# Performance work log

Hardware: AMD Instinct MI355X
Metric: run time of the kernel (lower is better)

## Reference

```python
import jax, jax.numpy as jnp
import numpy as np
from jax import lax

P = 8  # DFFN patch_size


def _ln(x, w, b):
    # WithBias LayerNorm over channel dim of NCHW (matches to_3d -> LN(-1) -> to_4d)
    mu = x.mean(1, keepdims=True)
    var = ((x - mu) ** 2).mean(1, keepdims=True)
    return (x - mu) / jnp.sqrt(var + 1e-5) * w[None, :, None, None] + b[None, :, None, None]


def _conv1x1(x, w, b=None):
    y = jnp.einsum('bchw,oc->bohw', x, w)
    if b is not None:
        y = y + b[None, :, None, None]
    return y


def setup_inputs() -> dict:
    key = jax.random.key(0)
    ks = jax.random.split(key, 9)
    B, C, H, W = 2, 64, 96, 96
    hid = C  # ffn_expansion_factor = 1
    s = lambda k, shape, scale=0.05: jax.random.normal(k, shape, jnp.float32) * scale
    return {
        'x': s(ks[0], (B, C, H, W), 1.0),
        'ln1_w': jnp.ones((C,), jnp.float32), 'ln1_b': jnp.zeros((C,), jnp.float32),
        'ln2_w': jnp.ones((C,), jnp.float32), 'ln2_b': jnp.zeros((C,), jnp.float32),
        'q_w': s(ks[1], (C, C)), 'q_b': jnp.zeros((C,), jnp.float32),
        'k_w': s(ks[2], (C, C)), 'k_b': jnp.zeros((C,), jnp.float32),
        'v_w': s(ks[3], (C, C)), 'v_b': jnp.zeros((C,), jnp.float32),
        'fft_w': s(ks[4], (hid, P, P // 2 + 1), 1.0),
        'proj_in_w': s(ks[5], (hid, C)),
        'dw_w': s(ks[6], (hid, 1, 3, 3)),
        'proj_out_w': s(ks[7], (C, hid // 2)),
    }


def reference(x, ln1_w, ln1_b, ln2_w, ln2_b, q_w, q_b, k_w, k_b, v_w, v_b,
              fft_w, proj_in_w, dw_w, proj_out_w):
    B, C, H, W = x.shape
    # --- attention sub-block (unscaled spatial self-attn) ---
    xn = _ln(x, ln1_w, ln1_b)
    q = _conv1x1(xn, q_w, q_b).reshape(B, C, H * W)
    k = _conv1x1(xn, k_w, k_b).reshape(B, C, H * W)
    v = _conv1x1(xn, v_w, v_b).reshape(B, C, H * W)
    attn = jax.nn.softmax(jnp.einsum('bcn,bcm->bnm', q, k), axis=-1)  # [B, HW, HW]
    out = jnp.einsum('bcm,bnm->bcn', v, attn).reshape(B, C, H, W)
    x = x + out
    # --- DFFN sub-block ---
    xn = _ln(x, ln2_w, ln2_b)
    h = _conv1x1(xn, proj_in_w)  # hidden == C (expansion factor 1)
    hid = h.shape[1]
    hb, wb = H // P, W // P
    hp = h.reshape(B, hid, hb, P, wb, P).transpose(0, 2, 4, 1, 3, 5)  # [B,hb,wb,hid,P,P]
    hf = jnp.fft.rfft2(hp) * fft_w  # real learned spectral filter
    hp = jnp.fft.irfft2(hf, s=(P, P))
    h = hp.transpose(0, 3, 1, 4, 2, 5).reshape(B, hid, H, W)
    h = lax.conv_general_dilated(h, dw_w, (1, 1), ((1, 1), (1, 1)),
                                 feature_group_count=hid,
                                 dimension_numbers=('NCHW', 'OIHW', 'NCHW'))
    h1, h2 = jnp.split(h, 2, axis=1)
    h = jax.nn.gelu(h1, approximate=False) * h2  # torch F.gelu is exact erf
    return x + _conv1x1(h, proj_out_w)
```

## Files before the change

kernel.cpp:

```cpp
#include <hip/hip_runtime.h>
#include <hip/hip_bf16.h>
#include <math.h>

#define CH 64
#define NPOS 9216
#define NTOT 18432
#define NSPLIT 12
#define TILES_PER_SPLIT 12
#define LOG2E 1.4426950408889634f

typedef short bf16x8 __attribute__((ext_vector_type(8)));
typedef short bf16x4 __attribute__((ext_vector_type(4)));
typedef float f32x4 __attribute__((ext_vector_type(4)));
typedef int   i32x4 __attribute__((ext_vector_type(4)));
typedef int   i32x2 __attribute__((ext_vector_type(2)));
typedef unsigned int u32;

__device__ __forceinline__ float bf2f(short s) {
  unsigned int u = ((unsigned int)(unsigned short)s) << 16;
  return __builtin_bit_cast(float, u);
}
__device__ __forceinline__ short f2bf(float f) {
  unsigned int u = __builtin_bit_cast(unsigned int, f);
  unsigned int r = (u + 0x7fffu + ((u >> 16) & 1u)) >> 16;
  return (short)r;
}
__device__ __forceinline__ float gelu_exact(float x) {
  return 0.5f * x * (1.f + erff(x * 0.70710678118654752440f));
}


__global__ __launch_bounds__(256) void k_ln_qkv(
    const float* __restrict__ x, const float* __restrict__ ln1w, const float* __restrict__ ln1b,
    const float* __restrict__ qw, const float* __restrict__ qb,
    const float* __restrict__ kw, const float* __restrict__ kb,
    const float* __restrict__ vw, const float* __restrict__ vb,
    short* __restrict__ Qg, short* __restrict__ Kg, short* __restrict__ Vgt) {
  int mat = blockIdx.y;
  int half = blockIdx.z;
  const float* wsrc = (mat == 0) ? qw : (mat == 1) ? kw : vw;
  const float* bsrc = (mat == 0) ? qb : (mat == 1) ? kb : vb;
  int idx = blockIdx.x * 256 + threadIdx.x;
  int b = idx / NPOS, n = idx % NPOS;
  const float* xb = x + (size_t)b * CH * NPOS + n;
  float xr[64];
  float mu = 0.f;
#pragma unroll
  for (int c = 0; c < 64; ++c) { float v = xb[c * NPOS]; xr[c] = v; mu += v; }
  mu *= (1.f / 64.f);
  float var = 0.f;
#pragma unroll
  for (int c = 0; c < 64; ++c) { float d = xr[c] - mu; var += d * d; }
  float rstd = rsqrtf(var * (1.f / 64.f) + 1e-5f);
#pragma unroll
  for (int c = 0; c < 64; ++c) xr[c] = (xr[c] - mu) * rstd * ln1w[c] + ln1b[c];
  if (mat == 2) {
    for (int o2 = 0; o2 < 4; ++o2) {
#pragma unroll
      for (int j = 0; j < 8; ++j) {
        int o = half * 32 + o2 * 8 + j;
        float acc = bsrc[o];
        const float* wrow = wsrc + o * 64;
#pragma unroll
        for (int c = 0; c < 64; ++c) acc += wrow[c] * xr[c];
        Vgt[(size_t)o * NTOT + idx] = f2bf(acc);
      }
    }
  } else {
    float kscale = (mat == 1) ? LOG2E : 1.f;
    short* outp = ((mat == 0) ? Qg : Kg) + (size_t)idx * 64 + half * 32;
    for (int o2 = 0; o2 < 4; ++o2) {
      bf16x8 v8;
#pragma unroll
      for (int j = 0; j < 8; ++j) {
        int o = half * 32 + o2 * 8 + j;
        float acc = bsrc[o];
        const float* wrow = wsrc + o * 64;
#pragma unroll
        for (int c = 0; c < 64; ++c) acc += wrow[c] * xr[c];
        v8[j] = f2bf(acc * kscale);
      }
      *(bf16x8*)(outp + o2 * 8) = v8;
    }
  }
}

#define LDPK 80
#define LDP  72
__global__ __launch_bounds__(512) void k_attn(
    const short* __restrict__ Qg, const short* __restrict__ Kg, const short* __restrict__ Vgt,
    u32* __restrict__ PoT, float* __restrict__ Pl) {
  __shared__ __align__(16) short Kt[2][64 * LDPK];
  __shared__ __align__(16) short Vt[2][64 * LDP];
  int b = blockIdx.y;
  int n0 = blockIdx.x * 256;
  int ks = blockIdx.z;
  int tid = threadIdx.x;
  int w = tid >> 6, lane = tid & 63;
  int L = lane & 15, quad = lane >> 4;

  bf16x8 qa[2][2];
#pragma unroll
  for (int qt = 0; qt < 2; ++qt) {
    const short* qb_ = Qg + ((size_t)(b * NPOS + n0 + w * 32 + qt * 16 + L)) * 64;
    qa[qt][0] = *(const bf16x8*)(qb_ + quad * 8);
    qa[qt][1] = *(const bf16x8*)(qb_ + 32 + quad * 8);
  }

  f32x4 o[2][4];
#pragma unroll
  for (int qt = 0; qt < 2; ++qt)
#pragma unroll
    for (int nb = 0; nb < 4; ++nb) o[qt][nb] = (f32x4){0.f, 0.f, 0.f, 0.f};
  float rl[2] = {0.f, 0.f};

  int ck = tid & 7, rk = tid >> 3;
  int c8 = tid & 7, dr = tid >> 3;
  int vslot = (c8 >> 2) * 32 + (c8 & 1) * 16 + ((c8 >> 1) & 1) * 4;
  i32x4 kr, vr;
  {
    int kt = ks * TILES_PER_SPLIT;
    kr = ((const i32x4*)(Kg + ((size_t)(b * NPOS + kt * 64)) * 64))[tid];
    vr = *(const i32x4*)(Vgt + (size_t)b * NPOS + kt * 64 + c8 * 8 + (size_t)dr * NTOT);
    ((i32x4*)Kt[0])[rk * 10 + ck] = kr;
    short* vrow = Vt[0] + dr * LDP + vslot;
    *(i32x2*)(vrow) = (i32x2){vr[0], vr[1]};
    *(i32x2*)(vrow + 8) = (i32x2){vr[2], vr[3]};
  }

  for (int t = 0; t < TILES_PER_SPLIT; ++t) {
    int cur = t & 1;
    if (t + 1 < TILES_PER_SPLIT) {
      int kt = ks * TILES_PER_SPLIT + t + 1;
      kr = ((const i32x4*)(Kg + ((size_t)(b * NPOS + kt * 64)) * 64))[tid];
      vr = *(const i32x4*)(Vgt + (size_t)b * NPOS + kt * 64 + c8 * 8 + (size_t)dr * NTOT);
    }
    __syncthreads();

    const i32x4* kt4 = (const i32x4*)Kt[cur];
    const short* vt = Vt[cur];
    __builtin_amdgcn_s_setprio(1);
#pragma unroll
    for (int kp = 0; kp < 2; ++kp) {
      u32 pw0[4], pw1[4];
#pragma unroll
      for (int h = 0; h < 2; ++h) {
        int kti = kp * 2 + h;
        bf16x8 kf0 = __builtin_bit_cast(bf16x8, kt4[(kti * 16 + L) * 10 + quad]);
        bf16x8 kf1 = __builtin_bit_cast(bf16x8, kt4[(kti * 16 + L) * 10 + 4 + quad]);
#pragma unroll
        for (int qt = 0; qt < 2; ++qt) {
          f32x4 st = {0.f, 0.f, 0.f, 0.f};
          st = __builtin_amdgcn_mfma_f32_16x16x32_bf16(kf0, qa[qt][0], st, 0, 0, 0);
          st = __builtin_amdgcn_mfma_f32_16x16x32_bf16(kf1, qa[qt][1], st, 0, 0, 0);
          float p0 = __builtin_amdgcn_exp2f(st[0]);
          float p1 = __builtin_amdgcn_exp2f(st[1]);
          float p2 = __builtin_amdgcn_exp2f(st[2]);
          float p3 = __builtin_amdgcn_exp2f(st[3]);
          rl[qt] += (p0 + p1) + (p2 + p3);
          u32 lo = __builtin_amdgcn_perm(__builtin_bit_cast(u32, p1), __builtin_bit_cast(u32, p0), 0x07060302u);
          u32 hi = __builtin_amdgcn_perm(__builtin_bit_cast(u32, p3), __builtin_bit_cast(u32, p2), 0x07060302u);
          if (qt == 0) { pw0[h * 2] = lo; pw0[h * 2 + 1] = hi; }
          else         { pw1[h * 2] = lo; pw1[h * 2 + 1] = hi; }
        }
      }
      i32x4 pq0 = {(int)pw0[0], (int)pw0[1], (int)pw0[2], (int)pw0[3]};
      i32x4 pq1 = {(int)pw1[0], (int)pw1[1], (int)pw1[2], (int)pw1[3]};
      bf16x8 pp0 = __builtin_bit_cast(bf16x8, pq0);
      bf16x8 pp1 = __builtin_bit_cast(bf16x8, pq1);
#pragma unroll
      for (int nb = 0; nb < 4; ++nb) {
        bf16x8 va8 = *(const bf16x8*)(vt + (nb * 16 + L) * LDP + kp * 32 + quad * 8);
        o[0][nb] = __builtin_amdgcn_mfma_f32_16x16x32_bf16(va8, pp0, o[0][nb], 0, 0, 0);
        o[1][nb] = __builtin_amdgcn_mfma_f32_16x16x32_bf16(va8, pp1, o[1][nb], 0, 0, 0);
      }
    }
    __builtin_amdgcn_s_setprio(0);

    if (t + 1 < TILES_PER_SPLIT) {
      int nxt = 1 - cur;
      ((i32x4*)Kt[nxt])[rk * 10 + ck] = kr;
      short* vrow = Vt[nxt] + dr * LDP + vslot;
      *(i32x2*)(vrow) = (i32x2){vr[0], vr[1]};
      *(i32x2*)(vrow + 8) = (i32x2){vr[2], vr[3]};
    }
  }

#pragma unroll
  for (int qt = 0; qt < 2; ++qt) {
    rl[qt] += __shfl_xor(rl[qt], 16);
    rl[qt] += __shfl_xor(rl[qt], 32);
  }

#pragma unroll
  for (int qt = 0; qt < 2; ++qt) {
    int qg = b * NPOS + n0 + w * 32 + qt * 16 + L;
#pragma unroll
    for (int nb = 0; nb < 4; ++nb)
#pragma unroll
      for (int ip = 0; ip < 2; ++ip) {
        u32 pk = ((u32)(unsigned short)f2bf(o[qt][nb][2 * ip + 1]) << 16) |
                 (u32)(unsigned short)f2bf(o[qt][nb][2 * ip]);
        int d32 = nb * 8 + quad * 2 + ip;
        PoT[((size_t)(ks * 32 + d32)) * NTOT + qg] = pk;
      }
    if (quad == 0) Pl[(size_t)ks * NTOT + qg] = rl[qt];
  }
}

__global__ __launch_bounds__(256) void k_res_ln2_proj(
    const float* __restrict__ x, const u32* __restrict__ PoT, const float* __restrict__ Pl,
    const float* __restrict__ ln2w, const float* __restrict__ ln2b,
    const float* __restrict__ piw,
    float* __restrict__ X2, float* __restrict__ Hbuf) {
  __shared__ float s1a[256], s2a[256];
  __shared__ __align__(16) short xn[32 * 72];
  int t = threadIdx.x;
  int w8 = t >> 5;
  int p = t & 31;
  int q0 = blockIdx.x * 32;
  int q = q0 + p;
  int b = q / NPOS;
  int nn = q0 % NPOS;
  int n = q % NPOS;

  float lsum = 0.f;
#pragma unroll
  for (int s = 0; s < NSPLIT; ++s) lsum += Pl[(size_t)s * NTOT + q];
  float inv = 1.f / lsum;

  const float* xb = x + (size_t)b * CH * NPOS + n;
  float xr[8];
  float s1 = 0.f, s2 = 0.f;
#pragma unroll
  for (int j2 = 0; j2 < 4; ++j2) {
    float a0 = 0.f, a1 = 0.f;
#pragma unroll
    for (int s = 0; s < NSPLIT; ++s) {
      u32 v = PoT[((size_t)(s * 32 + w8 * 4 + j2)) * NTOT + q];
      a0 += __builtin_bit_cast(float, v << 16);
      a1 += __builtin_bit_cast(float, v & 0xffff0000u);
    }
    int cl = 2 * j2;
    int c = w8 * 8 + cl;
    float v0 = xb[(size_t)c * NPOS] + a0 * inv;
    float v1 = xb[(size_t)(c + 1) * NPOS] + a1 * inv;
    xr[cl] = v0; xr[cl + 1] = v1;
    s1 += v0 + v1;
    s2 += v0 * v0 + v1 * v1;
  }
  s1a[w8 * 32 + p] = s1;
  s2a[w8 * 32 + p] = s2;
  {
    float* xo = X2 + (size_t)b * CH * NPOS + n;
#pragma unroll
    for (int cl = 0; cl < 8; ++cl) xo[(size_t)(w8 * 8 + cl) * NPOS] = xr[cl];
  }
  __syncthreads();
  float mu = 0.f, m2 = 0.f;
#pragma unroll
  for (int ww = 0; ww < 8; ++ww) { mu += s1a[ww * 32 + p]; m2 += s2a[ww * 32 + p]; }
  mu *= (1.f / 64.f);
  float var = m2 * (1.f / 64.f) - mu * mu;
  float rstd = rsqrtf(var + 1e-5f);
  {
    u32* xw = (u32*)xn;
#pragma unroll
    for (int j2 = 0; j2 < 4; ++j2) {
      int cl = 2 * j2, c = w8 * 8 + cl;
      float y0 = (xr[cl] - mu) * rstd * ln2w[c] + ln2b[c];
      float y1 = (xr[cl + 1] - mu) * rstd * ln2w[c + 1] + ln2b[c + 1];
      u32 pk = ((u32)(unsigned short)f2bf(y1) << 16) | (u32)(unsigned short)f2bf(y0);
      xw[p * 36 + w8 * 4 + j2] = pk;
    }
  }
  __syncthreads();
  int lane = t & 63;
  int L = lane & 15, quad = lane >> 4;
  int cs = t >> 6;
  bf16x8 a0, a1;
  {
    const float* wr = piw + (cs * 16 + L) * 64 + quad * 8;
#pragma unroll
    for (int j = 0; j < 8; ++j) { a0[j] = f2bf(wr[j]); a1[j] = f2bf(wr[32 + j]); }
  }
  float* hb = Hbuf + (size_t)b * CH * NPOS + nn;
#pragma unroll
  for (int ps = 0; ps < 2; ++ps) {
    bf16x8 b0 = *(const bf16x8*)(xn + (ps * 16 + L) * 72 + quad * 8);
    bf16x8 b1 = *(const bf16x8*)(xn + (ps * 16 + L) * 72 + 32 + quad * 8);
    f32x4 acc = {0.f, 0.f, 0.f, 0.f};
    acc = __builtin_amdgcn_mfma_f32_16x16x32_bf16(a0, b0, acc, 0, 0, 0);
    acc = __builtin_amdgcn_mfma_f32_16x16x32_bf16(a1, b1, acc, 0, 0, 0);
#pragma unroll
    for (int i = 0; i < 4; ++i)
      hb[(size_t)(cs * 16 + quad * 4 + i) * NPOS + ps * 16 + L] = acc[i];
  }
}

#define LDB 100
__global__ __launch_bounds__(96) void k_conv(
    float* __restrict__ Hbuf, const float* __restrict__ fftw) {
  __shared__ __align__(16) float band[8 * LDB];
  __shared__ float kl[64];
  int hb = blockIdx.x, c = blockIdx.y, b = blockIdx.z;
  int t = threadIdx.x;
  float* base = Hbuf + (size_t)(b * CH + c) * NPOS + hb * 8 * 96;
  if (t < 64) {
    int dp = t >> 3, dq = t & 7;
    const float r = 0.70710678118654752440f;
    const float CO[8] = {1.f, r, 0.f, -r, -1.f, -r, 0.f, r};
    const float* wc = fftw + c * 40;
    float acc = 0.f;
#pragma unroll
    for (int u = 0; u < 8; ++u) {
#pragma unroll
      for (int v = 0; v < 8; ++v) {
        float wv = (v <= 4) ? wc[u * 5 + v] : wc[((8 - u) & 7) * 5 + (8 - v)];
        acc += wv * CO[(u * dp + v * dq) & 7];
      }
    }
    kl[t] = acc * (1.f / 64.f);
  }
  {
    int sr = t / 12, sc = (t % 12) * 8;
    f32x4 a = *(const f32x4*)(base + sr * 96 + sc);
    f32x4 d = *(const f32x4*)(base + sr * 96 + sc + 4);
    *(f32x4*)&band[sr * LDB + sc] = a;
    *(f32x4*)&band[sr * LDB + sc + 4] = d;
  }
  __syncthreads();
  int p = t / 12, wb = t % 12;
  float out[8] = {0.f, 0.f, 0.f, 0.f, 0.f, 0.f, 0.f, 0.f};
#pragma unroll
  for (int dp = 0; dp < 8; ++dp) {
    int rr = (p - dp) & 7;
    f32x4 a = *(const f32x4*)&band[rr * LDB + wb * 8];
    f32x4 d = *(const f32x4*)&band[rr * LDB + wb * 8 + 4];
    float v[8] = {a[0], a[1], a[2], a[3], d[0], d[1], d[2], d[3]};
    const float* krow = &kl[dp * 8];
#pragma unroll
    for (int dq = 0; dq < 8; ++dq) {
      float kv = krow[dq];
#pragma unroll
      for (int q = 0; q < 8; ++q) out[q] += kv * v[(q - dq) & 7];
    }
  }
  __syncthreads();
  f32x4 w0 = {out[0], out[1], out[2], out[3]};
  f32x4 w1 = {out[4], out[5], out[6], out[7]};
  *(f32x4*)(base + p * 96 + wb * 8) = w0;
  *(f32x4*)(base + p * 96 + wb * 8 + 4) = w1;
}

__global__ __launch_bounds__(256) void k_dw_gate(
    const float* __restrict__ Hbuf, const float* __restrict__ dww,
    float* __restrict__ G) {
  int cc = blockIdx.y;
  int q = blockIdx.x * 256 + threadIdx.x;
  int b = q / NPOS, n = q % NPOS;
  int y = n / 96, xx = n % 96;
  const float* h1 = Hbuf + (size_t)(b * CH + cc) * NPOS;
  const float* h2 = Hbuf + (size_t)(b * CH + cc + 32) * NPOS;
  float wd1[9], wd2[9];
#pragma unroll
  for (int ki = 0; ki < 9; ++ki) { wd1[ki] = dww[cc * 9 + ki]; wd2[ki] = dww[(cc + 32) * 9 + ki]; }
  float d1 = 0.f, d2 = 0.f;
  for (int dy = -1; dy <= 1; ++dy) {
    int yy = y + dy;
    if (yy < 0 || yy >= 96) continue;
    for (int dx = -1; dx <= 1; ++dx) {
      int xv = xx + dx;
      if (xv < 0 || xv >= 96) continue;
      int ki = (dy + 1) * 3 + (dx + 1);
      d1 += h1[yy * 96 + xv] * wd1[ki];
      d2 += h2[yy * 96 + xv] * wd2[ki];
    }
  }
  G[(size_t)cc * NTOT + q] = gelu_exact(d1) * d2;
}

__global__ __launch_bounds__(256) void k_proj_out(
    const float* __restrict__ G, const float* __restrict__ poww,
    const float* __restrict__ X2, float* __restrict__ out) {
  int og = blockIdx.y;
  int q = blockIdx.x * 256 + threadIdx.x;
  int b = q / NPOS, n = q % NPOS;
  float g[32];
#pragma unroll
  for (int cg = 0; cg < 32; ++cg) g[cg] = G[(size_t)cg * NTOT + q];
  const float* xr = X2 + (size_t)b * CH * NPOS + n;
  float* ob = out + (size_t)b * CH * NPOS + n;
#pragma unroll
  for (int j = 0; j < 4; ++j) {
    int oc = og * 4 + j;
    const float* prow = poww + oc * 32;
    float acc = xr[(size_t)oc * NPOS];
#pragma unroll
    for (int cg = 0; cg < 32; ++cg) acc += prow[cg] * g[cg];
    ob[(size_t)oc * NPOS] = acc;
  }
}

extern "C" void kernel_launch(void* const* d_in, const int* in_sizes, int n_in,
                              void* d_out, int out_size, void* d_ws, size_t ws_size,
                              hipStream_t stream) {
  const float* x    = (const float*)d_in[0];
  const float* ln1w = (const float*)d_in[1];
  const float* ln1b = (const float*)d_in[2];
  const float* ln2w = (const float*)d_in[3];
  const float* ln2b = (const float*)d_in[4];
  const float* qw   = (const float*)d_in[5];
  const float* qb   = (const float*)d_in[6];
  const float* kw   = (const float*)d_in[7];
  const float* kb   = (const float*)d_in[8];
  const float* vw   = (const float*)d_in[9];
  const float* vb   = (const float*)d_in[10];
  const float* fftw = (const float*)d_in[11];
  const float* piw  = (const float*)d_in[12];
  const float* dww  = (const float*)d_in[13];
  const float* poww = (const float*)d_in[14];

  short* Qg  = (short*)d_ws;
  short* Kg  = Qg + (size_t)NTOT * 64;
  short* Vgt = Kg + (size_t)NTOT * 64;
  u32*   PoT = (u32*)(Vgt + (size_t)NTOT * 64);
  float* Pl  = (float*)(PoT + (size_t)NSPLIT * 32 * NTOT);
  float* X2  = Pl + (size_t)NSPLIT * NTOT;
  float* Hbuf = X2 + (size_t)NTOT * 64;
  float* G   = Hbuf + (size_t)NTOT * 64;

  k_ln_qkv<<<dim3(72, 3, 2), 256, 0, stream>>>(x, ln1w, ln1b, qw, qb, kw, kb, vw, vb, Qg, Kg, Vgt);
  k_attn<<<dim3(36, 2, NSPLIT), 512, 0, stream>>>(Qg, Kg, Vgt, PoT, Pl);
  k_res_ln2_proj<<<dim3(576), 256, 0, stream>>>(x, PoT, Pl, ln2w, ln2b, piw, X2, Hbuf);
  k_conv<<<dim3(12, 64, 2), 96, 0, stream>>>(Hbuf, fftw);
  k_dw_gate<<<dim3(72, 32), 256, 0, stream>>>(Hbuf, dww, G);
  k_proj_out<<<dim3(72, 16), 256, 0, stream>>>(G, poww, X2, (float*)d_out);
}
```

Baseline: 191.2 us.

## Compute LN1 and QKV projection with bf16 MFMA over 32-position tiles

```diff
diff --git a/kernel.cpp b/kernel.cpp
--- a/kernel.cpp
+++ b/kernel.cpp
@@ -36,51 +36,89 @@
     const float* __restrict__ kw, const float* __restrict__ kb,
     const float* __restrict__ vw, const float* __restrict__ vb,
     short* __restrict__ Qg, short* __restrict__ Kg, short* __restrict__ Vgt) {
-  int mat = blockIdx.y;
-  int half = blockIdx.z;
-  const float* wsrc = (mat == 0) ? qw : (mat == 1) ? kw : vw;
-  const float* bsrc = (mat == 0) ? qb : (mat == 1) ? kb : vb;
-  int idx = blockIdx.x * 256 + threadIdx.x;
-  int b = idx / NPOS, n = idx % NPOS;
+  __shared__ float s1a[256], s2a[256];
+  __shared__ __align__(16) short xn[32 * 72];
+  int t = threadIdx.x;
+  int w8 = t >> 5;
+  int p = t & 31;
+  int q0 = blockIdx.x * 32;
+  int q = q0 + p;
+  int b = q / NPOS;
+  int nn = q0 % NPOS;
+  int n = q % NPOS;
+
   const float* xb = x + (size_t)b * CH * NPOS + n;
-  float xr[64];
-  float mu = 0.f;
-#pragma unroll
-  for (int c = 0; c < 64; ++c) { float v = xb[c * NPOS]; xr[c] = v; mu += v; }
+  float xr[8];
+  float s1 = 0.f, s2 = 0.f;
+#pragma unroll
+  for (int cl = 0; cl < 8; ++cl) {
+    float v = xb[(size_t)(w8 * 8 + cl) * NPOS];
+    xr[cl] = v;
+    s1 += v;
+    s2 += v * v;
+  }
+  s1a[w8 * 32 + p] = s1;
+  s2a[w8 * 32 + p] = s2;
+  __syncthreads();
+  float mu = 0.f, m2 = 0.f;
+#pragma unroll
+  for (int ww = 0; ww < 8; ++ww) { mu += s1a[ww * 32 + p]; m2 += s2a[ww * 32 + p]; }
   mu *= (1.f / 64.f);
-  float var = 0.f;
-#pragma unroll
-  for (int c = 0; c < 64; ++c) { float d = xr[c] - mu; var += d * d; }
-  float rstd = rsqrtf(var * (1.f / 64.f) + 1e-5f);
-#pragma unroll
-  for (int c = 0; c < 64; ++c) xr[c] = (xr[c] - mu) * rstd * ln1w[c] + ln1b[c];
-  if (mat == 2) {
-    for (int o2 = 0; o2 < 4; ++o2) {
-#pragma unroll
-      for (int j = 0; j < 8; ++j) {
-        int o = half * 32 + o2 * 8 + j;
-        float acc = bsrc[o];
-        const float* wrow = wsrc + o * 64;
-#pragma unroll
-        for (int c = 0; c < 64; ++c) acc += wrow[c] * xr[c];
-        Vgt[(size_t)o * NTOT + idx] = f2bf(acc);
+  float var = m2 * (1.f / 64.f) - mu * mu;
+  float rstd = rsqrtf(var + 1e-5f);
+  {
+    u32* xw = (u32*)xn;
+#pragma unroll
+    for (int j2 = 0; j2 < 4; ++j2) {
+      int cl = 2 * j2, c = w8 * 8 + cl;
+      float y0 = (xr[cl] - mu) * rstd * ln1w[c] + ln1b[c];
+      float y1 = (xr[cl + 1] - mu) * rstd * ln1w[c + 1] + ln1b[c + 1];
+      u32 pk = ((u32)(unsigned short)f2bf(y1) << 16) | (u32)(unsigned short)f2bf(y0);
+      xw[p * 36 + w8 * 4 + j2] = pk;
+    }
+  }
+  __syncthreads();
+  int lane = t & 63;
+  int L = lane & 15, quad = lane >> 4;
+  int cs = t >> 6;
+  bf16x8 b0[2], b1[2];
+#pragma unroll
+  for (int ps = 0; ps < 2; ++ps) {
+    b0[ps] = *(const bf16x8*)(xn + (ps * 16 + L) * 72 + quad * 8);
+    b1[ps] = *(const bf16x8*)(xn + (ps * 16 + L) * 72 + 32 + quad * 8);
+  }
+#pragma unroll
+  for (int m = 0; m < 3; ++m) {
+    const float* wsrc = (m == 0) ? qw : (m == 1) ? kw : vw;
+    const float* bsrc = (m == 0) ? qb : (m == 1) ? kb : vb;
+    bf16x8 a0, a1;
+    {
+      const float* wr = wsrc + (cs * 16 + L) * 64 + quad * 8;
+#pragma unroll
+      for (int j = 0; j < 8; ++j) { a0[j] = f2bf(wr[j]); a1[j] = f2bf(wr[32 + j]); }
+    }
+    float bi[4];
+#pragma unroll
+    for (int i = 0; i < 4; ++i) bi[i] = bsrc[cs * 16 + quad * 4 + i];
+#pragma unroll
+    for (int ps = 0; ps < 2; ++ps) {
+      f32x4 acc = {bi[0], bi[1], bi[2], bi[3]};
+      acc = __builtin_amdgcn_mfma_f32_16x16x32_bf16(a0, b0[ps], acc, 0, 0, 0);
+      acc = __builtin_amdgcn_mfma_f32_16x16x32_bf16(a1, b1[ps], acc, 0, 0, 0);
+      int idx = b * NPOS + nn + ps * 16 + L;
+      if (m == 0) {
+#pragma unroll
+        for (int i = 0; i < 4; ++i)
+          Qg[(size_t)idx * 64 + cs * 16 + quad * 4 + i] = f2bf(acc[i]);
+      } else if (m == 1) {
+#pragma unroll
+        for (int i = 0; i < 4; ++i)
+          Kg[(size_t)idx * 64 + cs * 16 + quad * 4 + i] = f2bf(acc[i] * LOG2E);
+      } else {
+#pragma unroll
+        for (int i = 0; i < 4; ++i)
+          Vgt[(size_t)(cs * 16 + quad * 4 + i) * NTOT + idx] = f2bf(acc[i]);
       }
-    }
-  } else {
-    float kscale = (mat == 1) ? LOG2E : 1.f;
-    short* outp = ((mat == 0) ? Qg : Kg) + (size_t)idx * 64 + half * 32;
-    for (int o2 = 0; o2 < 4; ++o2) {
-      bf16x8 v8;
-#pragma unroll
-      for (int j = 0; j < 8; ++j) {
-        int o = half * 32 + o2 * 8 + j;
-        float acc = bsrc[o];
-        const float* wrow = wsrc + o * 64;
-#pragma unroll
-        for (int c = 0; c < 64; ++c) acc += wrow[c] * xr[c];
-        v8[j] = f2bf(acc * kscale);
-      }
-      *(bf16x8*)(outp + o2 * 8) = v8;
     }
   }
 }
@@ -430,7 +468,7 @@
   float* Hbuf = X2 + (size_t)NTOT * 64;
   float* G   = Hbuf + (size_t)NTOT * 64;
 
-  k_ln_qkv<<<dim3(72, 3, 2), 256, 0, stream>>>(x, ln1w, ln1b, qw, qb, kw, kb, vw, vb, Qg, Kg, Vgt);
+  k_ln_qkv<<<dim3(576), 256, 0, stream>>>(x, ln1w, ln1b, qw, qb, kw, kb, vw, vb, Qg, Kg, Vgt);
   k_attn<<<dim3(36, 2, NSPLIT), 512, 0, stream>>>(Qg, Kg, Vgt, PoT, Pl);
   k_res_ln2_proj<<<dim3(576), 256, 0, stream>>>(x, PoT, Pl, ln2w, ln2b, piw, X2, Hbuf);
   k_conv<<<dim3(12, 64, 2), 96, 0, stream>>>(Hbuf, fftw);
```

After: 170.6 us. 1.12x faster.
